# Performance work log

Hardware: AMD Instinct MI355X
Metric: run time of the kernel (lower is better)

## Reference

```python
import jax, jax.numpy as jnp
import numpy as np

B, I, O, G = 4096, 256, 256, 16


def setup_inputs() -> dict:
    key = jax.random.key(0)
    k1, k2 = jax.random.split(key)
    x = jax.random.normal(k1, (B, I), dtype=jnp.float32)
    # xavier_uniform bound for fan_in=I*G (last dim), fan_out=O treated per torch default on 4D: use small scale
    bound = float(np.sqrt(6.0 / (I * G + O * G)))
    laplacecoeffs = jax.random.uniform(k2, (2, O, I, G), dtype=jnp.float32, minval=-bound, maxval=bound)
    bias = jnp.zeros((1, O), dtype=jnp.float32)
    return {"x": x, "laplacecoeffs": laplacecoeffs, "bias": bias}


def reference(x, laplacecoeffs, bias):
    # x: (B, I); laplacecoeffs: (2, O, I, G); bias: (1, O)
    g = laplacecoeffs.shape[-1]  # static gridsize (clamped/rounded gridsize_param at init)
    lambdas = jnp.linspace(0.1, 1.0, g).astype(x.dtype)  # (G,)
    e = x[:, :, None] * lambdas  # (B, I, G)
    exp_neg = jnp.exp(-e)
    exp_pos = jnp.exp(e)
    # contract over (inputdim, gridsize) without materializing (B, O, I, G)
    y = jnp.einsum('big,oig->bo', exp_neg, laplacecoeffs[0])
    y = y + jnp.einsum('big,oig->bo', exp_pos, laplacecoeffs[1])
    y = y + bias  # (B, O)
    return y
```

## Files before the change

### kernel.cpp

```cpp
#include <hip/hip_runtime.h>


typedef __bf16 bf16x8 __attribute__((ext_vector_type(8)));
typedef __bf16 bf16x4 __attribute__((ext_vector_type(4)));
typedef float  f32x4  __attribute__((ext_vector_type(4)));

#define M_TOT 4096
#define N_TOT 256
#define MN_TOT (M_TOT * N_TOT)
#define SPLITK 8

__device__ __forceinline__ void gload_lds16(const __bf16* g, __bf16* l) {
  __builtin_amdgcn_global_load_lds(
      (const __attribute__((address_space(1))) void*)g,
      (__attribute__((address_space(3))) void*)l, 16, 0, 0);
}

__global__ void convert_w(const float* __restrict__ C, __bf16* __restrict__ W) {
  int t = blockIdx.x * 256 + threadIdx.x;
  int E = t << 2;
  int c = E >> 12, x4 = E & 4095;
  int s = c >> 8, o = c & 255;
  const f32x4 v = *(const f32x4*)(C + (size_t)c * 4096 + x4);
  bf16x4 w;
  w[0] = (__bf16)v[0]; w[1] = (__bf16)v[1]; w[2] = (__bf16)v[2]; w[3] = (__bf16)v[3];
  *(bf16x4*)(W + (size_t)o * 8192 + (size_t)s * 4096 + x4) = w;
}

template <int MODE>
__global__ __launch_bounds__(256, 2)
void laplace_gemm(const float* __restrict__ X, const __bf16* __restrict__ Wb,
                  const float* __restrict__ Bias, float* __restrict__ Out,
                  float* __restrict__ P) {
  __shared__ __bf16 As[128 * 72];
  __shared__ __bf16 Bs[128 * 64];

  const int tid = threadIdx.x;
  const int mt = blockIdx.x, nt = blockIdx.y, kt = blockIdx.z;
  const int m0 = mt * 128, n0 = nt * 128;
  const int s   = kt >> 2;
  const int i0c = (kt & 3) * 64;

  const int wv = tid >> 6, lane = tid & 63;
  const int wm = wv & 1, wn = wv >> 1;
  const int lm = lane & 15, q = lane >> 4;

  const int mr0 = tid >> 2,         ii0 = tid & 3;
  const int mr1 = (256 + tid) >> 2, ii1 = tid & 3;
  const float* xp0 = X + (size_t)(m0 + mr0) * 256 + i0c + ii0;
  const float* xp1 = X + (size_t)(m0 + mr1) * 256 + i0c + ii1;

  const float sgn = s ? 1.0f : -1.0f;
  const float c0 = 0.1f * sgn, cd = 0.06f * sgn;

  const f32x4 zero = {0.f, 0.f, 0.f, 0.f};
  f32x4 acc[4][4];
#pragma unroll
  for (int a = 0; a < 4; ++a)
#pragma unroll
    for (int b = 0; b < 4; ++b) acc[a][b] = zero;

  const size_t wrow = (size_t)s * 4096 + (size_t)i0c * 16;

  float xc0 = *xp0, xc1 = *xp1;

  for (int j = 0; j < 16; ++j) {
    const size_t kw = wrow + (size_t)j * 64;
#pragma unroll
    for (int qq = 0; qq < 4; ++qq) {
      const int idx = qq * 256 + tid;
      const int r = idx >> 3, cc = idx & 7;
      const __bf16* gsrc = Wb + (size_t)(n0 + r) * 8192 + kw + ((cc ^ (r & 7)) << 3);
      __bf16* ldst = Bs + ((qq * 256 + (tid & ~63)) << 3);
      gload_lds16(gsrc, ldst);
    }

    float xn0 = 0.f, xn1 = 0.f;
    if (j < 15) { xn0 = xp0[4 * (j + 1)]; xn1 = xp1[4 * (j + 1)]; }

    {
      const float p0 = __expf(c0 * xc0), rr = __expf(cd * xc0);
      bf16x8 v0, v1; float f = p0;
#pragma unroll
      for (int h = 0; h < 8; ++h) { v0[h] = (__bf16)f; f *= rr; }
#pragma unroll
      for (int h = 0; h < 8; ++h) { v1[h] = (__bf16)f; f *= rr; }
      *(bf16x8*)&As[mr0 * 72 + ii0 * 16]     = v0;
      *(bf16x8*)&As[mr0 * 72 + ii0 * 16 + 8] = v1;
    }
    {
      const float p0 = __expf(c0 * xc1), rr = __expf(cd * xc1);
      bf16x8 v0, v1; float f = p0;
#pragma unroll
      for (int h = 0; h < 8; ++h) { v0[h] = (__bf16)f; f *= rr; }
#pragma unroll
      for (int h = 0; h < 8; ++h) { v1[h] = (__bf16)f; f *= rr; }
      *(bf16x8*)&As[mr1 * 72 + ii1 * 16]     = v0;
      *(bf16x8*)&As[mr1 * 72 + ii1 * 16 + 8] = v1;
    }

    __syncthreads();

#pragma unroll
    for (int kk = 0; kk < 2; ++kk) {
      bf16x8 af[4], bf[4];
#pragma unroll
      for (int a = 0; a < 4; ++a)
        af[a] = *(const bf16x8*)&As[(wm * 64 + a * 16 + lm) * 72 + kk * 32 + q * 8];
      const int pc8 = (((kk << 2) + q) ^ (lm & 7)) << 3;
#pragma unroll
      for (int b = 0; b < 4; ++b)
        bf[b] = *(const bf16x8*)&Bs[(wn * 64 + b * 16 + lm) * 64 + pc8];
#pragma unroll
      for (int a = 0; a < 4; ++a)
#pragma unroll
        for (int b = 0; b < 4; ++b)
          acc[a][b] = __builtin_amdgcn_mfma_f32_16x16x32_bf16(af[a], bf[b], acc[a][b], 0, 0, 0);
    }
    __syncthreads();

    xc0 = xn0; xc1 = xn1;
  }

  if constexpr (MODE == 0) {
    float* Pk = P + (size_t)kt * MN_TOT;
#pragma unroll
    for (int a = 0; a < 4; ++a) {
      const int mrow = m0 + wm * 64 + a * 16 + q * 4;
#pragma unroll
      for (int rr = 0; rr < 4; ++rr)
#pragma unroll
        for (int b = 0; b < 4; ++b) {
          const int n = n0 + wn * 64 + b * 16 + lm;
          Pk[(size_t)(mrow + rr) * 256 + n] = acc[a][b][rr];
        }
    }
  } else {
#pragma unroll
    for (int a = 0; a < 4; ++a) {
      const int mrow = m0 + wm * 64 + a * 16 + q * 4;
#pragma unroll
      for (int rr = 0; rr < 4; ++rr)
#pragma unroll
        for (int b = 0; b < 4; ++b) {
          const int n = n0 + wn * 64 + b * 16 + lm;
          float v = acc[a][b][rr];
          if (kt == 0) v += Bias[n];
          atomicAdd(&Out[(size_t)(mrow + rr) * 256 + n], v);
        }
    }
  }
}

__global__ void reduce_bias(const float* __restrict__ P, const float* __restrict__ Bias,
                            float* __restrict__ Out) {
  const int t = blockIdx.x * 256 + threadIdx.x;
  const size_t base = (size_t)t * 4;
  f32x4 sv = *(const f32x4*)&P[base];
#pragma unroll
  for (int k = 1; k < SPLITK; ++k) sv += *(const f32x4*)&P[(size_t)k * MN_TOT + base];
  sv += *(const f32x4*)&Bias[base & 255];
  *(f32x4*)&Out[base] = sv;
}

extern "C" void kernel_launch(void* const* d_in, const int* in_sizes, int n_in,
                              void* d_out, int out_size, void* d_ws, size_t ws_size,
                              hipStream_t stream) {
  const float* X    = (const float*)d_in[0];
  const float* C    = (const float*)d_in[1];
  const float* Bias = (const float*)d_in[2];
  float* Out = (float*)d_out;

  __bf16* Wb = (__bf16*)d_ws;
  const size_t wb_bytes = (size_t)N_TOT * 8192 * sizeof(__bf16);
  const size_t p_bytes  = (size_t)SPLITK * MN_TOT * sizeof(float);
  float* P = (float*)((char*)d_ws + wb_bytes);

  convert_w<<<2048, 256, 0, stream>>>(C, Wb);

  if (ws_size >= wb_bytes + p_bytes) {
    laplace_gemm<0><<<dim3(32, 2, SPLITK), 256, 0, stream>>>(X, Wb, Bias, Out, P);
    reduce_bias<<<1024, 256, 0, stream>>>(P, Bias, Out);
  } else {
    hipMemsetAsync(d_out, 0, (size_t)out_size * sizeof(float), stream);
    laplace_gemm<1><<<dim3(32, 2, SPLITK), 256, 0, stream>>>(X, Wb, Bias, Out, P);
  }
}
```

Measured before the change: 92.47 us.

## Generate A fragments in registers and double-buffer B tiles in LDS

Drops the shared-memory A tile. Each lane now computes its exp-based bf16 A fragment directly in registers from vector loads of X, right before the MFMAs. The B weight tile is double-buffered so the async global-to-LDS load of the next k-step overlaps compute on the current one, leaving one barrier per iteration instead of two. In exchange, the exp work is duplicated across the two wn waves and X is reloaded redundantly per lane, which raises register pressure.

```diff
diff --git a/kernel.cpp b/kernel.cpp
--- a/kernel.cpp
+++ b/kernel.cpp
@@ -32,8 +32,7 @@
 void laplace_gemm(const float* __restrict__ X, const __bf16* __restrict__ Wb,
                   const float* __restrict__ Bias, float* __restrict__ Out,
                   float* __restrict__ P) {
-  __shared__ __bf16 As[128 * 72];
-  __shared__ __bf16 Bs[128 * 64];
+  __shared__ __bf16 Bs[2][128 * 64];
 
   const int tid = threadIdx.x;
   const int mt = blockIdx.x, nt = blockIdx.y, kt = blockIdx.z;
@@ -44,14 +43,17 @@
   const int wv = tid >> 6, lane = tid & 63;
   const int wm = wv & 1, wn = wv >> 1;
   const int lm = lane & 15, q = lane >> 4;
-
-  const int mr0 = tid >> 2,         ii0 = tid & 3;
-  const int mr1 = (256 + tid) >> 2, ii1 = tid & 3;
-  const float* xp0 = X + (size_t)(m0 + mr0) * 256 + i0c + ii0;
-  const float* xp1 = X + (size_t)(m0 + mr1) * 256 + i0c + ii1;
+  const int qh = q >> 1;
+  const int g0 = (q & 1) * 8;
 
   const float sgn = s ? 1.0f : -1.0f;
-  const float c0 = 0.1f * sgn, cd = 0.06f * sgn;
+  const float cd = 0.06f * sgn;
+  const float cl = sgn * (0.1f + 0.06f * (float)g0);
+
+  const float* xrow[4];
+#pragma unroll
+  for (int a = 0; a < 4; ++a)
+    xrow[a] = X + (size_t)(m0 + wm * 64 + a * 16 + lm) * 256 + i0c;
 
   const f32x4 zero = {0.f, 0.f, 0.f, 0.f};
   f32x4 acc[4][4];
@@ -62,64 +64,55 @@
 
   const size_t wrow = (size_t)s * 4096 + (size_t)i0c * 16;
 
-  float xc0 = *xp0, xc1 = *xp1;
-
-  for (int j = 0; j < 16; ++j) {
+  auto STAGE = [&](int j, int buf) {
     const size_t kw = wrow + (size_t)j * 64;
 #pragma unroll
     for (int qq = 0; qq < 4; ++qq) {
       const int idx = qq * 256 + tid;
       const int r = idx >> 3, cc = idx & 7;
       const __bf16* gsrc = Wb + (size_t)(n0 + r) * 8192 + kw + ((cc ^ (r & 7)) << 3);
-      __bf16* ldst = Bs + ((qq * 256 + (tid & ~63)) << 3);
+      __bf16* ldst = &Bs[buf][0] + ((qq * 256 + (tid & ~63)) << 3);
       gload_lds16(gsrc, ldst);
     }
+  };
 
-    float xn0 = 0.f, xn1 = 0.f;
-    if (j < 15) { xn0 = xp0[4 * (j + 1)]; xn1 = xp1[4 * (j + 1)]; }
+  STAGE(0, 0);
+  __syncthreads();
 
-    {
-      const float p0 = __expf(c0 * xc0), rr = __expf(cd * xc0);
-      bf16x8 v0, v1; float f = p0;
+  for (int j = 0; j < 16; ++j) {
+    const int cb = j & 1;
+    if (j < 15) STAGE(j + 1, cb ^ 1);
+
+    f32x4 xv[4];
 #pragma unroll
-      for (int h = 0; h < 8; ++h) { v0[h] = (__bf16)f; f *= rr; }
+    for (int a = 0; a < 4; ++a)
+      xv[a] = *(const f32x4*)(xrow[a] + 4 * j);
+
+    bf16x8 bfr[2][4];
 #pragma unroll
-      for (int h = 0; h < 8; ++h) { v1[h] = (__bf16)f; f *= rr; }
-      *(bf16x8*)&As[mr0 * 72 + ii0 * 16]     = v0;
-      *(bf16x8*)&As[mr0 * 72 + ii0 * 16 + 8] = v1;
+    for (int kk = 0; kk < 2; ++kk) {
+      const int pc8 = (((kk << 2) + q) ^ (lm & 7)) << 3;
+#pragma unroll
+      for (int b = 0; b < 4; ++b)
+        bfr[kk][b] = *(const bf16x8*)&Bs[cb][(wn * 64 + b * 16 + lm) * 64 + pc8];
     }
-    {
-      const float p0 = __expf(c0 * xc1), rr = __expf(cd * xc1);
-      bf16x8 v0, v1; float f = p0;
+
 #pragma unroll
-      for (int h = 0; h < 8; ++h) { v0[h] = (__bf16)f; f *= rr; }
+    for (int kk = 0; kk < 2; ++kk) {
 #pragma unroll
-      for (int h = 0; h < 8; ++h) { v1[h] = (__bf16)f; f *= rr; }
-      *(bf16x8*)&As[mr1 * 72 + ii1 * 16]     = v0;
-      *(bf16x8*)&As[mr1 * 72 + ii1 * 16 + 8] = v1;
+      for (int a = 0; a < 4; ++a) {
+        const float x  = qh ? xv[a][2 * kk + 1] : xv[a][2 * kk];
+        const float p0 = __expf(x * cl), rr = __expf(x * cd);
+        bf16x8 af; float f = p0;
+#pragma unroll
+        for (int h = 0; h < 8; ++h) { af[h] = (__bf16)f; f *= rr; }
+#pragma unroll
+        for (int b = 0; b < 4; ++b)
+          acc[a][b] = __builtin_amdgcn_mfma_f32_16x16x32_bf16(af, bfr[kk][b], acc[a][b], 0, 0, 0);
+      }
     }
 
     __syncthreads();
-
-#pragma unroll
-    for (int kk = 0; kk < 2; ++kk) {
-      bf16x8 af[4], bf[4];
-#pragma unroll
-      for (int a = 0; a < 4; ++a)
-        af[a] = *(const bf16x8*)&As[(wm * 64 + a * 16 + lm) * 72 + kk * 32 + q * 8];
-      const int pc8 = (((kk << 2) + q) ^ (lm & 7)) << 3;
-#pragma unroll
-      for (int b = 0; b < 4; ++b)
-        bf[b] = *(const bf16x8*)&Bs[(wn * 64 + b * 16 + lm) * 64 + pc8];
-#pragma unroll
-      for (int a = 0; a < 4; ++a)
-#pragma unroll
-        for (int b = 0; b < 4; ++b)
-          acc[a][b] = __builtin_amdgcn_mfma_f32_16x16x32_bf16(af[a], bf[b], acc[a][b], 0, 0, 0);
-    }
-    __syncthreads();
-
-    xc0 = xn0; xc1 = xn1;
   }
 
   if constexpr (MODE == 0) {
```

Measured after the change: 95.84 us. 3.6% more time.

## Double-buffer LDS tiles to overlap next-stage loads and exp generation with MFMA

Applied to the files above, without the earlier changes.

Splits the A and B shared-memory tiles into two buffers. Each iteration now issues the async global-to-LDS weight copy and computes the exp-generated A tile for step j+1 into the other buffer, then runs the MFMAs on the current buffer. This removes one barrier per iteration and lets memory latency and the exp math overlap with matrix work. In exchange, LDS use doubles to about 69 KB per block, which may reduce occupancy under launch_bounds(256,2), and the x loads are no longer prefetched a step ahead.

```diff
diff --git a/kernel.cpp b/kernel.cpp
--- a/kernel.cpp
+++ b/kernel.cpp
@@ -32,8 +32,8 @@
 void laplace_gemm(const float* __restrict__ X, const __bf16* __restrict__ Wb,
                   const float* __restrict__ Bias, float* __restrict__ Out,
                   float* __restrict__ P) {
-  __shared__ __bf16 As[128 * 72];
-  __shared__ __bf16 Bs[128 * 64];
+  __shared__ __bf16 As[2][128 * 72];
+  __shared__ __bf16 Bs[2][128 * 64];
 
   const int tid = threadIdx.x;
   const int mt = blockIdx.x, nt = blockIdx.y, kt = blockIdx.z;
@@ -45,10 +45,10 @@
   const int wm = wv & 1, wn = wv >> 1;
   const int lm = lane & 15, q = lane >> 4;
 
-  const int mr0 = tid >> 2,         ii0 = tid & 3;
-  const int mr1 = (256 + tid) >> 2, ii1 = tid & 3;
-  const float* xp0 = X + (size_t)(m0 + mr0) * 256 + i0c + ii0;
-  const float* xp1 = X + (size_t)(m0 + mr1) * 256 + i0c + ii1;
+  const int mr0 = tid >> 2, ii = tid & 3;
+  const int mr1 = 64 + mr0;
+  const float* xp0 = X + (size_t)(m0 + mr0) * 256 + i0c + ii;
+  const float* xp1 = X + (size_t)(m0 + mr1) * 256 + i0c + ii;
 
   const float sgn = s ? 1.0f : -1.0f;
   const float c0 = 0.1f * sgn, cd = 0.06f * sgn;
@@ -62,64 +62,68 @@
 
   const size_t wrow = (size_t)s * 4096 + (size_t)i0c * 16;
 
-  float xc0 = *xp0, xc1 = *xp1;
-
-  for (int j = 0; j < 16; ++j) {
+  auto STAGE = [&](int j, int buf) {
     const size_t kw = wrow + (size_t)j * 64;
 #pragma unroll
     for (int qq = 0; qq < 4; ++qq) {
       const int idx = qq * 256 + tid;
       const int r = idx >> 3, cc = idx & 7;
       const __bf16* gsrc = Wb + (size_t)(n0 + r) * 8192 + kw + ((cc ^ (r & 7)) << 3);
-      __bf16* ldst = Bs + ((qq * 256 + (tid & ~63)) << 3);
+      __bf16* ldst = &Bs[buf][0] + ((qq * 256 + (tid & ~63)) << 3);
       gload_lds16(gsrc, ldst);
     }
+  };
 
-    float xn0 = 0.f, xn1 = 0.f;
-    if (j < 15) { xn0 = xp0[4 * (j + 1)]; xn1 = xp1[4 * (j + 1)]; }
-
+  auto GENA = [&](int j, int buf) {
+    const float x0 = xp0[4 * j], x1 = xp1[4 * j];
     {
-      const float p0 = __expf(c0 * xc0), rr = __expf(cd * xc0);
+      const float p0 = __expf(c0 * x0), rr = __expf(cd * x0);
       bf16x8 v0, v1; float f = p0;
 #pragma unroll
       for (int h = 0; h < 8; ++h) { v0[h] = (__bf16)f; f *= rr; }
 #pragma unroll
       for (int h = 0; h < 8; ++h) { v1[h] = (__bf16)f; f *= rr; }
-      *(bf16x8*)&As[mr0 * 72 + ii0 * 16]     = v0;
-      *(bf16x8*)&As[mr0 * 72 + ii0 * 16 + 8] = v1;
+      *(bf16x8*)&As[buf][mr0 * 72 + ii * 16]     = v0;
+      *(bf16x8*)&As[buf][mr0 * 72 + ii * 16 + 8] = v1;
     }
     {
-      const float p0 = __expf(c0 * xc1), rr = __expf(cd * xc1);
+      const float p0 = __expf(c0 * x1), rr = __expf(cd * x1);
       bf16x8 v0, v1; float f = p0;
 #pragma unroll
       for (int h = 0; h < 8; ++h) { v0[h] = (__bf16)f; f *= rr; }
 #pragma unroll
       for (int h = 0; h < 8; ++h) { v1[h] = (__bf16)f; f *= rr; }
-      *(bf16x8*)&As[mr1 * 72 + ii1 * 16]     = v0;
-      *(bf16x8*)&As[mr1 * 72 + ii1 * 16 + 8] = v1;
+      *(bf16x8*)&As[buf][mr1 * 72 + ii * 16]     = v0;
+      *(bf16x8*)&As[buf][mr1 * 72 + ii * 16 + 8] = v1;
     }
+  };
 
-    __syncthreads();
+  STAGE(0, 0);
+  GENA(0, 0);
+  __syncthreads();
+
+  for (int j = 0; j < 16; ++j) {
+    const int cb = j & 1;
+    if (j < 15) { STAGE(j + 1, cb ^ 1); GENA(j + 1, cb ^ 1); }
 
 #pragma unroll
     for (int kk = 0; kk < 2; ++kk) {
-      bf16x8 af[4], bf[4];
+      bf16x8 af[4], bfr[4];
 #pragma unroll
       for (int a = 0; a < 4; ++a)
-        af[a] = *(const bf16x8*)&As[(wm * 64 + a * 16 + lm) * 72 + kk * 32 + q * 8];
+        af[a] = *(const bf16x8*)&As[cb][(wm * 64 + a * 16 + lm) * 72 + kk * 32 + q * 8];
       const int pc8 = (((kk << 2) + q) ^ (lm & 7)) << 3;
 #pragma unroll
       for (int b = 0; b < 4; ++b)
-        bf[b] = *(const bf16x8*)&Bs[(wn * 64 + b * 16 + lm) * 64 + pc8];
+        bfr[b] = *(const bf16x8*)&Bs[cb][(wn * 64 + b * 16 + lm) * 64 + pc8];
 #pragma unroll
       for (int a = 0; a < 4; ++a)
 #pragma unroll
         for (int b = 0; b < 4; ++b)
-          acc[a][b] = __builtin_amdgcn_mfma_f32_16x16x32_bf16(af[a], bf[b], acc[a][b], 0, 0, 0);
+          acc[a][b] = __builtin_amdgcn_mfma_f32_16x16x32_bf16(af[a], bfr[b], acc[a][b], 0, 0, 0);
     }
-    __syncthreads();
 
-    xc0 = xn0; xc1 = xn1;
+    if (j < 15) __syncthreads();
   }
 
   if constexpr (MODE == 0) {
```

After: 93.67 us. About the same (+1.3%).
